# Performance work log

Hardware: AMD Instinct MI355X
Metric: run time of the kernel (lower is better)

## Reference

```python
import jax, jax.numpy as jnp
import numpy as np

M = 23          # number of dendritic subunits
N_SYN = 1500    # number of synapses
T = 30000       # timesteps
B = 101         # temporal kernel length (odd -> 'same' output length)
G_NO = 4        # synapse groups (first half excitatory double-exp kernel)
PAD = B // 2
# parent (1-based) of each subunit; 0 marks root; children have higher index
C_DEN = np.array([0] + [((m - 1) // 2) + 1 for m in range(1, M)], dtype=np.int64)
G_ASSIGN = np.arange(N_SYN, dtype=np.int64) % G_NO   # synapse -> group
SYN_SUB = np.arange(N_SYN, dtype=np.int64) % M       # synapse -> subunit (C_syn nonzeros)


def setup_inputs() -> dict:
    key = jax.random.key(0)
    X = jax.random.uniform(key, (T, N_SYN), dtype=jnp.float32)
    V_o = jnp.ones((1,), jnp.float32) * -69.0
    Tau = jnp.ones((G_NO,), jnp.float32) * 1.4
    Delta = jnp.ones((1,), jnp.float32) * 0.25
    W = jnp.concatenate([jnp.full((G_NO // 2,), 2.0, jnp.float32),
                         jnp.full((G_NO - G_NO // 2,), -1.0, jnp.float32)]) * 0.05
    C = jnp.ones((M,), jnp.float32)
    Theta = jnp.zeros((M,), jnp.float32)
    return {"X": X, "V_o": V_o, "Tau": Tau, "Delta": Delta, "W": W, "C": C, "Theta": Theta}


def _group_kernels(Tau, Delta):
    # shared shifted time base, clamped at 0
    t = jnp.maximum(jnp.arange(B, dtype=jnp.float32) - jnp.exp(Delta[0]), 0.0)  # [B]
    tau = jnp.exp(Tau)[:, None]                               # [G_NO, 1]
    tf = t[None, :] / tau
    fast = tf * jnp.exp(-tf)                                   # alpha kernel
    ts = t[None, :] / (tau * 2.8 + 10.4)
    slow = ts * jnp.exp(-ts) * 0.3
    exc = (fast + slow) / 1.3                                  # dual-exp for excitatory groups
    is_exc = (jnp.arange(G_NO) < G_NO // 2)[:, None]
    return jnp.where(is_exc, exc, fast)                        # [G_NO, B]


def _forward(X, V_o, Tau, Delta, W, C, Theta):
    kern = _group_kernels(Tau, Delta)                          # [G_NO, B]
    g = jnp.asarray(G_ASSIGN)
    # conv is linear, so fold the per-group weight W[g] into the kernel
    k_syn = kern[g] * W[g][:, None]                            # [N_SYN, B]
    # depthwise cross-correlation (matches torch F.conv1d), 'same' padding
    filt = jax.lax.conv_general_dilated(
        X.T[None],                 # [1, N, T]
        k_syn[:, None, :],         # [N, 1, B]
        window_strides=(1,), padding=[(PAD, PAD)],
        feature_group_count=N_SYN,
        dimension_numbers=('NCH', 'OIH', 'NCH'))[0].T          # [T, N]
    # gather-sum of synapses into subunits (C_syn sign only selects membership)
    A = jax.nn.one_hot(jnp.asarray(SYN_SUB), M, dtype=X.dtype)  # [N, M]
    sub_in = filt @ A                                           # [T, M]
    expC = jnp.exp(C)
    # internal nodes processed from leaves toward root (descending indices)
    roots = (np.flip(np.unique(C_DEN))[:-1] - 1).astype(int)
    root_set = set(roots.tolist())
    out = [None] * M
    for m in range(M):                                          # leaves
        if m not in root_set:
            out[m] = jax.nn.sigmoid(sub_in[:, m] - Theta[m]) * expC[m]
    for r in roots:                                             # tree reduction
        s = sub_in[:, r]
        for k in np.where(C_DEN == r + 1)[0]:
            s = s + out[k]
        out[r] = jax.nn.sigmoid(s - Theta[r]) * expC[r]
    return out[0] + V_o[0]                                      # [T]


def reference(X, V_o, Tau, Delta, W, C, Theta):
    return _forward(X, V_o, Tau, Delta, W, C, Theta)
```

## Files before the change

### kernel.cpp

```cpp
#include <hip/hip_runtime.h>
#include <cstddef>

#define T_DIM 30000
#define M_DIM 23
#define NJ    92
#define TILE  64
#define STR   184
#define SUBS  25
#define XP4   377
#define WPS   144

typedef short bf16x8 __attribute__((ext_vector_type(8)));
typedef float f32x4  __attribute__((ext_vector_type(4)));

__device__ __forceinline__ unsigned short f2bf(float f) {
    unsigned int u = __float_as_uint(f);
    return (unsigned short)((u + 0x7fffu + ((u >> 16) & 1u)) >> 16);
}

__global__ __launch_bounds__(128) void reduce_k(const float* __restrict__ X,
                                                unsigned short* __restrict__ Yb) {
    __shared__ __align__(16) float4 Xs[2 * XP4];

    const int tid = threadIdx.x;
    const int tb  = blockIdx.x * 2;

    const float4* Xg = reinterpret_cast<const float4*>(X) + (size_t)tb * 375;
    #pragma unroll
    for (int it = 0; it < 6; ++it) {
        int i = tid + 128 * it;
        if (i < 750) {
            int r = (i >= 375) ? 1 : 0;
            int pos = i - r * 375;
            Xs[r * XP4 + pos] = Xg[i];
        }
    }
    __syncthreads();

    if (tid < 46) {
        int r = tid / 23;
        int q = tid - 23 * r;
        const float4* row = &Xs[r * XP4];
        float4 s = make_float4(0.f, 0.f, 0.f, 0.f);
        #pragma unroll
        for (int k = 0; k < 16; ++k) {
            float4 v = row[q + 23 * k];
            s.x += v.x; s.y += v.y; s.z += v.z; s.w += v.w;
        }
        if (q < 7) {
            float4 v = row[q + 23 * 16];
            s.x += v.x; s.y += v.y; s.z += v.z; s.w += v.w;
        }
        ushort4 o;
        o.x = f2bf(s.x); o.y = f2bf(s.y); o.z = f2bf(s.z); o.w = f2bf(s.w);
        reinterpret_cast<ushort4*>(Yb)[(size_t)(tb + r) * 23 + q] = o;
    }
}

__global__ __launch_bounds__(512, 2) void conv_tree_k(
    const unsigned short* __restrict__ Yb,
    const float* __restrict__ Tau,
    const float* __restrict__ Delta,
    const float* __restrict__ W,
    const float* __restrict__ Vo,
    const float* __restrict__ C,
    const float* __restrict__ Theta,
    float* __restrict__ out)
{
    __shared__ __align__(16) unsigned short Yt[NJ * STR];
    __shared__ __align__(16) float wpadT[4 * WPS];
    __shared__ float sub[TILE * SUBS];
    __shared__ float sTheta[M_DIM];
    __shared__ float sExpC[M_DIM];

    const int tid = threadIdx.x;
    const int t0  = blockIdx.x * TILE;
    const int l   = tid & 63;

    {
        float eD = __expf(Delta[0]);
        for (int i = tid; i < 4 * WPS; i += 512) {
            int g = i / WPS;
            int x = (i - g * WPS) - 16;
            float val = 0.f;
            if (x >= 0 && x <= 100) {
                float tt  = fmaxf((float)x - eD, 0.f);
                float tau = __expf(Tau[g]);
                float tf  = tt / tau;
                float fast = tf * __expf(-tf);
                float kv;
                if (g < 2) {
                    float ts = tt / (tau * 2.8f + 10.4f);
                    kv = (fast + ts * __expf(-ts) * 0.3f) * (1.0f / 1.3f);
                } else {
                    kv = fast;
                }
                val = kv * W[g];
            }
            wpadT[i] = val;
        }
    }
    if (tid < M_DIM) {
        sTheta[tid] = Theta[tid];
        sExpC[tid]  = __expf(C[tid]);
    }
    __syncthreads();

    {
        unsigned int* Yw = reinterpret_cast<unsigned int*>(Yt);
        for (int i = tid; i < 88 * 23; i += 512) {
            int rp = i / 23;
            int q  = i - rp * 23;
            int g0 = t0 - 50 + 2 * rp;
            ushort4 ra = make_ushort4(0, 0, 0, 0);
            ushort4 rb = make_ushort4(0, 0, 0, 0);
            if ((unsigned)g0       < (unsigned)T_DIM) ra = reinterpret_cast<const ushort4*>(Yb)[(size_t)g0 * 23 + q];
            if ((unsigned)(g0 + 1) < (unsigned)T_DIM) rb = reinterpret_cast<const ushort4*>(Yb)[(size_t)(g0 + 1) * 23 + q];
            Yw[(q     ) * 92 + rp] = (unsigned)ra.x | ((unsigned)rb.x << 16);
            Yw[(q + 23) * 92 + rp] = (unsigned)ra.y | ((unsigned)rb.y << 16);
            Yw[(q + 46) * 92 + rp] = (unsigned)ra.z | ((unsigned)rb.z << 16);
            Yw[(q + 69) * 92 + rp] = (unsigned)ra.w | ((unsigned)rb.w << 16);
        }
    }

    const int n  = l & 15;
    const int kq = (l >> 4) << 3;
    uint4 af[16];
    #pragma unroll
    for (int g = 0; g < 4; ++g) {
        const float* wp = &wpadT[g * WPS + 16 - n + kq];
        #pragma unroll
        for (int kk = 0; kk < 4; ++kk) {
            const float* wk8 = wp + kk * 32;
            unsigned int d[4];
            #pragma unroll
            for (int p = 0; p < 4; ++p) {
                unsigned short lo = f2bf(wk8[2 * p]);
                unsigned short hi = f2bf(wk8[2 * p + 1]);
                d[p] = (unsigned)lo | ((unsigned)hi << 16);
            }
            af[g * 4 + kk] = make_uint4(d[0], d[1], d[2], d[3]);
        }
    }

    const int wave = tid >> 6;
    const int dt   = (wave & 3) * 16;
    const int nt   = wave >> 2;
    const int m    = nt * 16 + n;
    const bool mvalid = (m < M_DIM);
    const int mc   = mvalid ? m : 0;

    __syncthreads();

    f32x4 acc = {0.f, 0.f, 0.f, 0.f};
    #pragma unroll
    for (int g = 0; g < 4; ++g) {
        int a  = (3 * ((g - mc) & 3)) & 3;
        int j  = mc + 23 * a;
        int cp = (j >> 2) + 23 * g;
        const unsigned short* colp = &Yt[cp * STR + dt + kq];

        bf16x8 b0 = *reinterpret_cast<const bf16x8*>(colp);
        acc = __builtin_amdgcn_mfma_f32_16x16x32_bf16(__builtin_bit_cast(bf16x8, af[g*4+0]), b0, acc, 0, 0, 0);
        bf16x8 b1 = *reinterpret_cast<const bf16x8*>(colp + 32);
        acc = __builtin_amdgcn_mfma_f32_16x16x32_bf16(__builtin_bit_cast(bf16x8, af[g*4+1]), b1, acc, 0, 0, 0);
        bf16x8 b2 = *reinterpret_cast<const bf16x8*>(colp + 64);
        acc = __builtin_amdgcn_mfma_f32_16x16x32_bf16(__builtin_bit_cast(bf16x8, af[g*4+2]), b2, acc, 0, 0, 0);
        bf16x8 b3 = *reinterpret_cast<const bf16x8*>(colp + 96);
        acc = __builtin_amdgcn_mfma_f32_16x16x32_bf16(__builtin_bit_cast(bf16x8, af[g*4+3]), b3, acc, 0, 0, 0);
    }

    if (mvalid) {
        int i0 = (l >> 4) * 4;
        #pragma unroll
        for (int r = 0; r < 4; ++r)
            sub[(dt + i0 + r) * SUBS + m] = acc[r];
    }
    __syncthreads();

    if (tid < TILE) {
        int t = t0 + tid;
        if (t < T_DIM) {
            const float* s = &sub[tid * SUBS];
            float o[M_DIM];
            #pragma unroll
            for (int mm = 11; mm < 23; ++mm) {
                float x = s[mm] - sTheta[mm];
                o[mm] = sExpC[mm] / (1.f + __expf(-x));
            }
            #pragma unroll
            for (int rr = 10; rr >= 0; --rr) {
                float x = s[rr] + o[2 * rr + 1] + o[2 * rr + 2] - sTheta[rr];
                o[rr] = sExpC[rr] / (1.f + __expf(-x));
            }
            out[t] = o[0] + Vo[0];
        }
    }
}

extern "C" void kernel_launch(void* const* d_in, const int* in_sizes, int n_in,
                              void* d_out, int out_size, void* d_ws, size_t ws_size,
                              hipStream_t stream) {
    const float* X     = (const float*)d_in[0];
    const float* Vo    = (const float*)d_in[1];
    const float* Tau   = (const float*)d_in[2];
    const float* Delta = (const float*)d_in[3];
    const float* W     = (const float*)d_in[4];
    const float* C     = (const float*)d_in[5];
    const float* Theta = (const float*)d_in[6];
    float* out = (float*)d_out;
    unsigned short* Yb = (unsigned short*)d_ws;

    reduce_k<<<T_DIM / 2, 128, 0, stream>>>(X, Yb);
    conv_tree_k<<<(T_DIM + TILE - 1) / TILE, 512, 0, stream>>>(
        Yb, Tau, Delta, W, Vo, C, Theta, out);
}
```

Measured before the change: 42.60 us.

## Write reduced inputs column-major padded so conv reads MFMA operands directly from global

The reduce kernel now writes the per-column bf16 sums into a transposed, zero-padded column-major workspace, with one row of T plus halo per column. The conv kernel can then load MFMA B operands straight from global memory, dropping the shared-memory transpose stage and one barrier. Both kernels also remap block indices across the 8 XCDs so neighbouring tiles share L2. The trade-off is scattered 4-byte writes in the reduce kernel and uncoalesced 16-byte global loads in the conv kernel.

```diff
diff --git a/kernel.cpp b/kernel.cpp
--- a/kernel.cpp
+++ b/kernel.cpp
@@ -5,10 +5,12 @@
 #define M_DIM 23
 #define NJ    92
 #define TILE  64
-#define STR   184
 #define SUBS  25
 #define XP4   377
 #define WPS   144
+#define PADC  50
+#define CSTR  30208
+#define CSTR32 (CSTR/2)
 
 typedef short bf16x8 __attribute__((ext_vector_type(8)));
 typedef float f32x4  __attribute__((ext_vector_type(4)));
@@ -18,12 +20,15 @@
     return (unsigned short)((u + 0x7fffu + ((u >> 16) & 1u)) >> 16);
 }
 
-__global__ __launch_bounds__(128) void reduce_k(const float* __restrict__ X,
-                                                unsigned short* __restrict__ Yb) {
+__global__ __launch_bounds__(128) void reduce_t(const float* __restrict__ X,
+                                                unsigned short* __restrict__ Ycp) {
     __shared__ __align__(16) float4 Xs[2 * XP4];
+    __shared__ unsigned short Ytr[92 * 2];
 
     const int tid = threadIdx.x;
-    const int tb  = blockIdx.x * 2;
+    const int b   = blockIdx.x;
+    const int swb = (b & 7) * 1875 + (b >> 3);
+    const int tb  = swb * 2;
 
     const float4* Xg = reinterpret_cast<const float4*>(X) + (size_t)tb * 375;
     #pragma unroll
@@ -51,14 +56,27 @@
             float4 v = row[q + 23 * 16];
             s.x += v.x; s.y += v.y; s.z += v.z; s.w += v.w;
         }
-        ushort4 o;
-        o.x = f2bf(s.x); o.y = f2bf(s.y); o.z = f2bf(s.z); o.w = f2bf(s.w);
-        reinterpret_cast<ushort4*>(Yb)[(size_t)(tb + r) * 23 + q] = o;
+        Ytr[(4 * q + 0) * 2 + r] = f2bf(s.x);
+        Ytr[(4 * q + 1) * 2 + r] = f2bf(s.y);
+        Ytr[(4 * q + 2) * 2 + r] = f2bf(s.z);
+        Ytr[(4 * q + 3) * 2 + r] = f2bf(s.w);
+    }
+    __syncthreads();
+
+    if (tid < 92) {
+        unsigned int v = (unsigned)Ytr[tid * 2] | ((unsigned)Ytr[tid * 2 + 1] << 16);
+        reinterpret_cast<unsigned int*>(Ycp)[(size_t)tid * CSTR32 + (PADC + tb) / 2] = v;
+    }
+
+    if (b < 92 && tid < 104) {
+        unsigned int* col32 = reinterpret_cast<unsigned int*>(Ycp) + (size_t)b * CSTR32;
+        int u = (tid < 25) ? tid : (15025 + (tid - 25));
+        col32[u] = 0u;
     }
 }
 
 __global__ __launch_bounds__(512, 2) void conv_tree_k(
-    const unsigned short* __restrict__ Yb,
+    const unsigned short* __restrict__ Ycp,
     const float* __restrict__ Tau,
     const float* __restrict__ Delta,
     const float* __restrict__ W,
@@ -67,14 +85,16 @@
     const float* __restrict__ Theta,
     float* __restrict__ out)
 {
-    __shared__ __align__(16) unsigned short Yt[NJ * STR];
     __shared__ __align__(16) float wpadT[4 * WPS];
     __shared__ float sub[TILE * SUBS];
     __shared__ float sTheta[M_DIM];
     __shared__ float sExpC[M_DIM];
 
     const int tid = threadIdx.x;
-    const int t0  = blockIdx.x * TILE;
+    const int bb  = blockIdx.x;
+    const int xcd = bb & 7, ii = bb >> 3;
+    const int wkid = (xcd < 5) ? (xcd * 59 + ii) : (295 + (xcd - 5) * 58 + ii);
+    const int t0  = wkid * TILE;
     const int l   = tid & 63;
 
     {
@@ -106,23 +126,6 @@
     }
     __syncthreads();
 
-    {
-        unsigned int* Yw = reinterpret_cast<unsigned int*>(Yt);
-        for (int i = tid; i < 88 * 23; i += 512) {
-            int rp = i / 23;
-            int q  = i - rp * 23;
-            int g0 = t0 - 50 + 2 * rp;
-            ushort4 ra = make_ushort4(0, 0, 0, 0);
-            ushort4 rb = make_ushort4(0, 0, 0, 0);
-            if ((unsigned)g0       < (unsigned)T_DIM) ra = reinterpret_cast<const ushort4*>(Yb)[(size_t)g0 * 23 + q];
-            if ((unsigned)(g0 + 1) < (unsigned)T_DIM) rb = reinterpret_cast<const ushort4*>(Yb)[(size_t)(g0 + 1) * 23 + q];
-            Yw[(q     ) * 92 + rp] = (unsigned)ra.x | ((unsigned)rb.x << 16);
-            Yw[(q + 23) * 92 + rp] = (unsigned)ra.y | ((unsigned)rb.y << 16);
-            Yw[(q + 46) * 92 + rp] = (unsigned)ra.z | ((unsigned)rb.z << 16);
-            Yw[(q + 69) * 92 + rp] = (unsigned)ra.w | ((unsigned)rb.w << 16);
-        }
-    }
-
     const int n  = l & 15;
     const int kq = (l >> 4) << 3;
     uint4 af[16];
@@ -150,15 +153,12 @@
     const bool mvalid = (m < M_DIM);
     const int mc   = mvalid ? m : 0;
 
-    __syncthreads();
-
     f32x4 acc = {0.f, 0.f, 0.f, 0.f};
     #pragma unroll
     for (int g = 0; g < 4; ++g) {
         int a  = (3 * ((g - mc) & 3)) & 3;
         int j  = mc + 23 * a;
-        int cp = (j >> 2) + 23 * g;
-        const unsigned short* colp = &Yt[cp * STR + dt + kq];
+        const unsigned short* colp = Ycp + (size_t)j * CSTR + t0 + dt + kq;
 
         bf16x8 b0 = *reinterpret_cast<const bf16x8*>(colp);
         acc = __builtin_amdgcn_mfma_f32_16x16x32_bf16(__builtin_bit_cast(bf16x8, af[g*4+0]), b0, acc, 0, 0, 0);
@@ -209,9 +209,8 @@
     const float* C     = (const float*)d_in[5];
     const float* Theta = (const float*)d_in[6];
     float* out = (float*)d_out;
-    unsigned short* Yb = (unsigned short*)d_ws;
-
-    reduce_k<<<T_DIM / 2, 128, 0, stream>>>(X, Yb);
-    conv_tree_k<<<(T_DIM + TILE - 1) / TILE, 512, 0, stream>>>(
-        Yb, Tau, Delta, W, Vo, C, Theta, out);
-}
+    unsigned short* Ycp = (unsigned short*)d_ws;
+
+    reduce_t<<<T_DIM / 2, 128, 0, stream>>>(X, Ycp);
+    conv_tree_k<<<469, 512, 0, stream>>>(Ycp, Tau, Delta, W, Vo, C, Theta, out);
+}
```

Result: slower. 43.57 us (+2.3%).
